# Kernel tuning notes

Measured on AMD Instinct MI355X. Metric: run time of the kernel, lower is better.

The kernel has to match this reference:

```python
import jax, jax.numpy as jnp
import numpy as np


def _base_grid(B, H, W, dtype):
    # Faithful to the original torch loops, including the (i-1) off-by-one:
    # base_grid[i, :, 0] = -1 + (i-1)/(H-1)*2   (row index in channel 0)
    # base_grid[:, j, 1] = -1 + (j-1)/(W-1)*2   (col index in channel 1)
    row = -1.0 + (jnp.arange(H, dtype=dtype) - 1.0) / (H - 1) * 2.0
    col = -1.0 + (jnp.arange(W, dtype=dtype) - 1.0) / (W - 1) * 2.0
    g = jnp.stack([jnp.broadcast_to(row[:, None], (H, W)),
                   jnp.broadcast_to(col[None, :], (H, W))], axis=-1)  # [H,W,2]
    return jnp.broadcast_to(g, (B, H, W, 2))


def _grid_sample(img, grid):
    # torch.nn.functional.grid_sample, bilinear, padding_mode='zeros', align_corners=True
    # img: [B,C,H,W]; grid: [B,Hg,Wg,2], grid[...,0]=x (width), grid[...,1]=y (height)
    B, C, H, W = img.shape
    Hg, Wg = grid.shape[1], grid.shape[2]
    x = (grid[..., 0] + 1.0) * 0.5 * (W - 1)  # [B,Hg,Wg]
    y = (grid[..., 1] + 1.0) * 0.5 * (H - 1)
    x0 = jnp.floor(x); y0 = jnp.floor(y)
    x1 = x0 + 1.0;     y1 = y0 + 1.0
    wx1 = x - x0; wx0 = 1.0 - wx1
    wy1 = y - y0; wy0 = 1.0 - wy1
    imgf = img.reshape(B, C, H * W)

    def gather(yy, xx):
        inb = ((yy >= 0) & (yy <= H - 1) & (xx >= 0) & (xx <= W - 1))
        yc = jnp.clip(yy, 0, H - 1).astype(jnp.int32)
        xc = jnp.clip(xx, 0, W - 1).astype(jnp.int32)
        lin = (yc * W + xc).reshape(B, 1, Hg * Wg)
        v = jnp.take_along_axis(imgf, jnp.broadcast_to(lin, (B, C, Hg * Wg)), axis=2)
        return v * inb.reshape(B, 1, Hg * Wg).astype(img.dtype)

    def w(a):
        return a.reshape(B, 1, Hg * Wg)

    out = (gather(y0, x0) * w(wy0 * wx0) + gather(y0, x1) * w(wy0 * wx1)
           + gather(y1, x0) * w(wy1 * wx0) + gather(y1, x1) * w(wy1 * wx1))
    return out.reshape(B, C, Hg, Wg)


def _warp(img, flow):
    B, _, H, W = flow.shape
    grid = _base_grid(B, H, W, img.dtype) + jnp.transpose(flow, (0, 2, 3, 1))
    return _grid_sample(img, grid)


def setup_inputs() -> dict:
    key = jax.random.key(0)
    B, C = 16, 16
    sizes = [512, 256, 128, 64]
    keys = jax.random.split(key, 8)
    inp = {}
    for i, s in enumerate(sizes):
        inp[f"img{i}"] = jax.random.normal(keys[2 * i], (B, C, s, s), dtype=jnp.float32)
        inp[f"flow{i}"] = jax.random.normal(keys[2 * i + 1], (B, 2, s, s), dtype=jnp.float32)
    return inp


def reference(img0, flow0, img1, flow1, img2, flow2, img3, flow3):
    return (_warp(img0, flow0), _warp(img1, flow1),
            _warp(img2, flow2), _warp(img3, flow3))
```

## Files before the change

kernel.cpp:

```cpp
#include <hip/hip_runtime.h>

typedef float f4 __attribute__((ext_vector_type(4)));

namespace {
constexpr int B = 16;
constexpr int C = 16;
}

template <int S>
__global__ __launch_bounds__(256) void transpose_kernel(
    const float* __restrict__ img, float* __restrict__ ws, int total)
{
    constexpr int SS = S * S;
    int idx = blockIdx.x * 256 + threadIdx.x;
    if (idx >= total) return;
    const int bb  = idx / SS;
    const int rem = idx - bb * SS;

    const float* ip = img + (size_t)bb * C * SS + rem;
    float v[C];
#pragma unroll
    for (int c = 0; c < C; ++c) v[c] = ip[(size_t)c * SS];

    f4* op = (f4*)(ws + (size_t)idx * C);
#pragma unroll
    for (int k = 0; k < C / 4; ++k) {
        f4 t = { v[4 * k + 0], v[4 * k + 1], v[4 * k + 2], v[4 * k + 3] };
        op[k] = t;
    }
}

template <int S>
__global__ __launch_bounds__(256) void gather_kernel(
    const float* __restrict__ ws, const float* __restrict__ flow,
    float* __restrict__ out, int total)
{
    constexpr int SS = S * S;
    int idx = blockIdx.x * 256 + threadIdx.x;
    if (idx >= total) return;
    const int bb  = idx / SS;
    const int rem = idx - bb * SS;
    const int i   = rem / S;
    const int j   = rem - i * S;

    const float f0 = flow[(size_t)bb * 2 * SS + rem];
    const float f1 = flow[(size_t)bb * 2 * SS + SS + rem];

    const float sm1 = (float)(S - 1);
    const float gx = -1.0f + ((float)i - 1.0f) / sm1 * 2.0f + f0;
    const float gy = -1.0f + ((float)j - 1.0f) / sm1 * 2.0f + f1;
    const float x = (gx + 1.0f) * 0.5f * sm1;
    const float y = (gy + 1.0f) * 0.5f * sm1;

    const float x0f = floorf(x), y0f = floorf(y);
    const float x1f = x0f + 1.0f, y1f = y0f + 1.0f;
    const float wx1 = x - x0f, wx0 = 1.0f - wx1;
    const float wy1 = y - y0f, wy0 = 1.0f - wy1;

    const bool bx0 = (x0f >= 0.0f) && (x0f <= sm1);
    const bool bx1 = (x1f >= 0.0f) && (x1f <= sm1);
    const bool by0 = (y0f >= 0.0f) && (y0f <= sm1);
    const bool by1 = (y1f >= 0.0f) && (y1f <= sm1);

    const int xc0 = (int)fminf(fmaxf(x0f, 0.0f), sm1);
    const int xc1 = (int)fminf(fmaxf(x1f, 0.0f), sm1);
    const int yc0 = (int)fminf(fmaxf(y0f, 0.0f), sm1);
    const int yc1 = (int)fminf(fmaxf(y1f, 0.0f), sm1);

    const float w00 = (by0 && bx0) ? wy0 * wx0 : 0.0f;
    const float w01 = (by0 && bx1) ? wy0 * wx1 : 0.0f;
    const float w10 = (by1 && bx0) ? wy1 * wx0 : 0.0f;
    const float w11 = (by1 && bx1) ? wy1 * wx1 : 0.0f;

    f4 a0 = {0.f, 0.f, 0.f, 0.f};
    f4 a1 = a0, a2 = a0, a3 = a0;

    const float* base = ws + (size_t)bb * SS * C;

    if (w00 != 0.0f || w01 != 0.0f) {
        const f4* p0 = (const f4*)(base + (size_t)(yc0 * S + xc0) * C);
        const f4* p1 = (const f4*)(base + (size_t)(yc0 * S + xc1) * C);
        a0 += w00 * p0[0] + w01 * p1[0];
        a1 += w00 * p0[1] + w01 * p1[1];
        a2 += w00 * p0[2] + w01 * p1[2];
        a3 += w00 * p0[3] + w01 * p1[3];
    }
    if (w10 != 0.0f || w11 != 0.0f) {
        const f4* p0 = (const f4*)(base + (size_t)(yc1 * S + xc0) * C);
        const f4* p1 = (const f4*)(base + (size_t)(yc1 * S + xc1) * C);
        a0 += w10 * p0[0] + w11 * p1[0];
        a1 += w10 * p0[1] + w11 * p1[1];
        a2 += w10 * p0[2] + w11 * p1[2];
        a3 += w10 * p0[3] + w11 * p1[3];
    }

    float* ob = out + (size_t)bb * C * SS + rem;
    f4 acc[4] = { a0, a1, a2, a3 };
#pragma unroll
    for (int k = 0; k < 4; ++k) {
#pragma unroll
        for (int e = 0; e < 4; ++e) {
            __builtin_nontemporal_store(acc[k][e], &ob[(size_t)(k * 4 + e) * SS]);
        }
    }
}

template <int S>
__global__ __launch_bounds__(256) void warp_fallback(
    const float* __restrict__ img, const float* __restrict__ flow,
    float* __restrict__ out, int total)
{
    constexpr int SS = S * S;
    int idx = blockIdx.x * 256 + threadIdx.x;
    if (idx >= total) return;
    const int b   = idx / SS;
    const int rem = idx - b * SS;
    const int i   = rem / S;
    const int j   = rem - i * S;

    const float f0 = flow[(size_t)b * 2 * SS + rem];
    const float f1 = flow[(size_t)b * 2 * SS + SS + rem];

    const float sm1 = (float)(S - 1);
    const float gx = -1.0f + ((float)i - 1.0f) / sm1 * 2.0f + f0;
    const float gy = -1.0f + ((float)j - 1.0f) / sm1 * 2.0f + f1;
    const float x = (gx + 1.0f) * 0.5f * sm1;
    const float y = (gy + 1.0f) * 0.5f * sm1;

    const float x0f = floorf(x), y0f = floorf(y);
    const float x1f = x0f + 1.0f, y1f = y0f + 1.0f;
    const float wx1 = x - x0f, wx0 = 1.0f - wx1;
    const float wy1 = y - y0f, wy0 = 1.0f - wy1;

    const bool bx0 = (x0f >= 0.0f) && (x0f <= sm1);
    const bool bx1 = (x1f >= 0.0f) && (x1f <= sm1);
    const bool by0 = (y0f >= 0.0f) && (y0f <= sm1);
    const bool by1 = (y1f >= 0.0f) && (y1f <= sm1);

    const int xc0 = (int)fminf(fmaxf(x0f, 0.0f), sm1);
    const int xc1 = (int)fminf(fmaxf(x1f, 0.0f), sm1);
    const int yc0 = (int)fminf(fmaxf(y0f, 0.0f), sm1);
    const int yc1 = (int)fminf(fmaxf(y1f, 0.0f), sm1);

    const float w00 = (by0 && bx0) ? wy0 * wx0 : 0.0f;
    const float w01 = (by0 && bx1) ? wy0 * wx1 : 0.0f;
    const float w10 = (by1 && bx0) ? wy1 * wx0 : 0.0f;
    const float w11 = (by1 && bx1) ? wy1 * wx1 : 0.0f;

    const int o00 = yc0 * S + xc0;
    const int o01 = yc0 * S + xc1;
    const int o10 = yc1 * S + xc0;
    const int o11 = yc1 * S + xc1;

    const float* ib = img + (size_t)b * C * SS;
    float*       ob = out + (size_t)b * C * SS + rem;

    if (w00 + w01 + w10 + w11 != 0.0f) {
#pragma unroll 4
        for (int c = 0; c < C; ++c) {
            const float* p = ib + (size_t)c * SS;
            ob[(size_t)c * SS] =
                w00 * p[o00] + w01 * p[o01] + w10 * p[o10] + w11 * p[o11];
        }
    } else {
#pragma unroll 4
        for (int c = 0; c < C; ++c) ob[(size_t)c * SS] = 0.0f;
    }
}

template <int S>
static void run_scale(const float* img, const float* flow, float* out,
                      float* ws, size_t ws_size, hipStream_t stream)
{
    constexpr int SS = S * S;
    const size_t per_b = (size_t)SS * C * sizeof(float);
    int chunk = (ws == nullptr) ? 0 : (int)(ws_size / per_b);
    if (chunk > B) chunk = B;

    if (chunk >= 1) {
        for (int b0 = 0; b0 < B; b0 += chunk) {
            const int nb    = (b0 + chunk <= B) ? chunk : (B - b0);
            const int total = nb * SS;
            const int grid  = (total + 255) / 256;
            transpose_kernel<S><<<grid, 256, 0, stream>>>(
                img + (size_t)b0 * C * SS, ws, total);
            gather_kernel<S><<<grid, 256, 0, stream>>>(
                ws, flow + (size_t)b0 * 2 * SS,
                out + (size_t)b0 * C * SS, total);
        }
    } else {
        const int total = B * SS;
        warp_fallback<S><<<(total + 255) / 256, 256, 0, stream>>>(
            img, flow, out, total);
    }
}

extern "C" void kernel_launch(void* const* d_in, const int* , int ,
                              void* d_out, int , void* d_ws, size_t ws_size,
                              hipStream_t stream)
{
    float* out = (float*)d_out;
    float* ws  = (float*)d_ws;

    run_scale<512>((const float*)d_in[0], (const float*)d_in[1], out, ws, ws_size, stream);
    out += (size_t)B * C * 512 * 512;
    run_scale<256>((const float*)d_in[2], (const float*)d_in[3], out, ws, ws_size, stream);
    out += (size_t)B * C * 256 * 256;
    run_scale<128>((const float*)d_in[4], (const float*)d_in[5], out, ws, ws_size, stream);
    out += (size_t)B * C * 128 * 128;
    run_scale<64>((const float*)d_in[6], (const float*)d_in[7], out, ws, ws_size, stream);
}
```

Before: 785.3 us.

## Split channels across four threads per pixel and chunk workspace to cache size

Each pixel's 16 channels are now handled by four threads, each covering one group of four channels, in both the transpose and gather kernels. This raises parallelism and cuts per-thread register and memory work. Image reads in the transpose kernel become nontemporal loads. The batch chunk is capped so that each workspace chunk is about 32 MB, aiming to keep the transposed image cache-resident between the transpose and gather kernels. In exchange there are more kernel launches, and the flow loads and coordinate math are repeated four times per pixel.

```diff
diff --git a/kernel.cpp b/kernel.cpp
--- a/kernel.cpp
+++ b/kernel.cpp
@@ -9,37 +9,37 @@
 
 template <int S>
 __global__ __launch_bounds__(256) void transpose_kernel(
-    const float* __restrict__ img, float* __restrict__ ws, int total)
-{
-    constexpr int SS = S * S;
-    int idx = blockIdx.x * 256 + threadIdx.x;
-    if (idx >= total) return;
-    const int bb  = idx / SS;
-    const int rem = idx - bb * SS;
-
-    const float* ip = img + (size_t)bb * C * SS + rem;
-    float v[C];
-#pragma unroll
-    for (int c = 0; c < C; ++c) v[c] = ip[(size_t)c * SS];
-
-    f4* op = (f4*)(ws + (size_t)idx * C);
-#pragma unroll
-    for (int k = 0; k < C / 4; ++k) {
-        f4 t = { v[4 * k + 0], v[4 * k + 1], v[4 * k + 2], v[4 * k + 3] };
-        op[k] = t;
-    }
+    const float* __restrict__ img, float* __restrict__ ws, int total4)
+{
+    constexpr int SS = S * S;
+    int t = blockIdx.x * 256 + threadIdx.x;
+    if (t >= total4) return;
+    const int q   = t & 3;
+    const int p   = t >> 2;
+    const int bb  = p / SS;
+    const int rem = p - bb * SS;
+
+    const float* ip = img + (size_t)bb * C * SS + (size_t)(4 * q) * SS + rem;
+    f4 v;
+    v.x = __builtin_nontemporal_load(&ip[0]);
+    v.y = __builtin_nontemporal_load(&ip[SS]);
+    v.z = __builtin_nontemporal_load(&ip[2 * SS]);
+    v.w = __builtin_nontemporal_load(&ip[3 * SS]);
+    *(f4*)(ws + (size_t)p * C + 4 * q) = v;
 }
 
 template <int S>
 __global__ __launch_bounds__(256) void gather_kernel(
     const float* __restrict__ ws, const float* __restrict__ flow,
-    float* __restrict__ out, int total)
-{
-    constexpr int SS = S * S;
-    int idx = blockIdx.x * 256 + threadIdx.x;
-    if (idx >= total) return;
-    const int bb  = idx / SS;
-    const int rem = idx - bb * SS;
+    float* __restrict__ out, int total4)
+{
+    constexpr int SS = S * S;
+    int t = blockIdx.x * 256 + threadIdx.x;
+    if (t >= total4) return;
+    const int q   = t & 3;
+    const int p   = t >> 2;
+    const int bb  = p / SS;
+    const int rem = p - bb * SS;
     const int i   = rem / S;
     const int j   = rem - i * S;
 
@@ -72,37 +72,25 @@
     const float w10 = (by1 && bx0) ? wy1 * wx0 : 0.0f;
     const float w11 = (by1 && bx1) ? wy1 * wx1 : 0.0f;
 
-    f4 a0 = {0.f, 0.f, 0.f, 0.f};
-    f4 a1 = a0, a2 = a0, a3 = a0;
-
-    const float* base = ws + (size_t)bb * SS * C;
+    const float* base = ws + (size_t)bb * SS * C + 4 * q;
+    f4 a = {0.f, 0.f, 0.f, 0.f};
 
     if (w00 != 0.0f || w01 != 0.0f) {
-        const f4* p0 = (const f4*)(base + (size_t)(yc0 * S + xc0) * C);
-        const f4* p1 = (const f4*)(base + (size_t)(yc0 * S + xc1) * C);
-        a0 += w00 * p0[0] + w01 * p1[0];
-        a1 += w00 * p0[1] + w01 * p1[1];
-        a2 += w00 * p0[2] + w01 * p1[2];
-        a3 += w00 * p0[3] + w01 * p1[3];
+        f4 t0 = *(const f4*)(base + (size_t)(yc0 * S + xc0) * C);
+        f4 t1 = *(const f4*)(base + (size_t)(yc0 * S + xc1) * C);
+        a += w00 * t0 + w01 * t1;
     }
     if (w10 != 0.0f || w11 != 0.0f) {
-        const f4* p0 = (const f4*)(base + (size_t)(yc1 * S + xc0) * C);
-        const f4* p1 = (const f4*)(base + (size_t)(yc1 * S + xc1) * C);
-        a0 += w10 * p0[0] + w11 * p1[0];
-        a1 += w10 * p0[1] + w11 * p1[1];
-        a2 += w10 * p0[2] + w11 * p1[2];
-        a3 += w10 * p0[3] + w11 * p1[3];
-    }
-
-    float* ob = out + (size_t)bb * C * SS + rem;
-    f4 acc[4] = { a0, a1, a2, a3 };
-#pragma unroll
-    for (int k = 0; k < 4; ++k) {
-#pragma unroll
-        for (int e = 0; e < 4; ++e) {
-            __builtin_nontemporal_store(acc[k][e], &ob[(size_t)(k * 4 + e) * SS]);
-        }
-    }
+        f4 t0 = *(const f4*)(base + (size_t)(yc1 * S + xc0) * C);
+        f4 t1 = *(const f4*)(base + (size_t)(yc1 * S + xc1) * C);
+        a += w10 * t0 + w11 * t1;
+    }
+
+    float* ob = out + (size_t)bb * C * SS + (size_t)(4 * q) * SS + rem;
+    __builtin_nontemporal_store(a.x, &ob[0]);
+    __builtin_nontemporal_store(a.y, &ob[SS]);
+    __builtin_nontemporal_store(a.z, &ob[2 * SS]);
+    __builtin_nontemporal_store(a.w, &ob[3 * SS]);
 }
 
 template <int S>
@@ -158,9 +146,9 @@
     if (w00 + w01 + w10 + w11 != 0.0f) {
 #pragma unroll 4
         for (int c = 0; c < C; ++c) {
-            const float* p = ib + (size_t)c * SS;
+            const float* pp = ib + (size_t)c * SS;
             ob[(size_t)c * SS] =
-                w00 * p[o00] + w01 * p[o01] + w10 * p[o10] + w11 * p[o11];
+                w00 * pp[o00] + w01 * pp[o01] + w10 * pp[o10] + w11 * pp[o11];
         }
     } else {
 #pragma unroll 4
@@ -174,19 +162,23 @@
 {
     constexpr int SS = S * S;
     const size_t per_b = (size_t)SS * C * sizeof(float);
-    int chunk = (ws == nullptr) ? 0 : (int)(ws_size / per_b);
+
+    int chunk = (int)((32u << 20) / per_b);
+    if (chunk < 1) chunk = 1;
     if (chunk > B) chunk = B;
+    if (ws == nullptr || ws_size < per_b) chunk = 0;
+    while (chunk >= 1 && (size_t)chunk * per_b > ws_size) chunk >>= 1;
 
     if (chunk >= 1) {
         for (int b0 = 0; b0 < B; b0 += chunk) {
-            const int nb    = (b0 + chunk <= B) ? chunk : (B - b0);
-            const int total = nb * SS;
-            const int grid  = (total + 255) / 256;
+            const int nb     = (b0 + chunk <= B) ? chunk : (B - b0);
+            const int total4 = nb * SS * 4;
+            const int grid   = (total4 + 255) / 256;
             transpose_kernel<S><<<grid, 256, 0, stream>>>(
-                img + (size_t)b0 * C * SS, ws, total);
+                img + (size_t)b0 * C * SS, ws, total4);
             gather_kernel<S><<<grid, 256, 0, stream>>>(
                 ws, flow + (size_t)b0 * 2 * SS,
-                out + (size_t)b0 * C * SS, total);
+                out + (size_t)b0 * C * SS, total4);
         }
     } else {
         const int total = B * SS;
```

Result: slower. 850.5 us (+8.3%).
